# Optimization experiments

Hardware: AMD Instinct MI355X
Metric: run time of the kernel (lower is better)

The kernel has to match this reference:

```python
import jax, jax.numpy as jnp
import numpy as np

EPS = 1e-8  # torch F.cosine_similarity eps


def setup_inputs() -> dict:
    key = jax.random.key(0)
    ks = jax.random.split(key, 5)
    S, Q, D_in, D, N_WAY, K_SHOT = 100, 4096, 21168, 64, 20, 5
    return {
        "support_images": jax.random.normal(ks[0], (S, D_in), dtype=jnp.float32),
        "support_labels": jax.random.randint(ks[1], (S,), 0, N_WAY),
        "query_images": jax.random.normal(ks[2], (Q, D_in), dtype=jnp.float32),
        "n_way": N_WAY,
        "k_shot": K_SHOT,
        "backbone_w": jax.random.normal(ks[3], (D_in, D), dtype=jnp.float32) * 0.02,
        "backbone_b": jax.random.normal(ks[4], (D,), dtype=jnp.float32) * 0.02,
    }


def _l2_normalize(x):
    # matches torch cosine_similarity: x / max(||x||, eps)
    n = jnp.maximum(jnp.linalg.norm(x, axis=-1, keepdims=True), EPS)
    return x / n


def reference(support_images, support_labels, query_images, n_way, k_shot,
              backbone_w, backbone_b):
    # Backbone: linear embedding (stand-in for conv feature extractor)
    support_emb = support_images @ backbone_w + backbone_b   # [S, D]
    query_emb = query_images @ backbone_w + backbone_b       # [Q, D]

    # Cosine similarity between every query and every support sample: [Q, S]
    sims = _l2_normalize(query_emb) @ _l2_normalize(support_emb).T

    # Softmax over the support axis (per query), as in the original loop
    attn = jax.nn.softmax(sims, axis=1)                      # [Q, S]

    # Per-label scatter-add == one-hot segment-sum: [Q, n_way]
    one_hot = jax.nn.one_hot(support_labels, n_way, dtype=attn.dtype)  # [S, n_way]
    logits = attn @ one_hot
    return logits
```

## Files before the change

kernel.cpp:

```cpp
#include <hip/hip_runtime.h>
#include <hip/hip_bf16.h>
#include <math.h>

#define DEMB 64
#define BM   64
#define BKF  64
#define KSMAX 16

using short8 = __attribute__((ext_vector_type(8))) short;
using u16x8  = __attribute__((ext_vector_type(8))) unsigned short;
using f32x4  = __attribute__((ext_vector_type(4))) float;

__device__ __forceinline__ u16x8 cvt_bf8(float4 a0, float4 a1) {
    union { u16x8 s; __hip_bfloat16 h[8]; } u;
    u.h[0] = __float2bfloat16(a0.x);
    u.h[1] = __float2bfloat16(a0.y);
    u.h[2] = __float2bfloat16(a0.z);
    u.h[3] = __float2bfloat16(a0.w);
    u.h[4] = __float2bfloat16(a1.x);
    u.h[5] = __float2bfloat16(a1.y);
    u.h[6] = __float2bfloat16(a1.z);
    u.h[7] = __float2bfloat16(a1.w);
    return u.s;
}

__device__ __forceinline__ void gl16(const void* gsrc, void* lds) {
    __builtin_amdgcn_global_load_lds(
        (const __attribute__((address_space(1))) unsigned int*)gsrc,
        (__attribute__((address_space(3))) unsigned int*)lds,
        16, 0, 0);
}

__global__ __launch_bounds__(256) void prep_wt(
    const float* __restrict__ W, unsigned short* __restrict__ Wtk, int Din)
{
    const int t = blockIdx.x * 256 + threadIdx.x;
    const int oct = t >> 6, c = t & 63;
    union { u16x8 v; __hip_bfloat16 h[8]; } u;
    #pragma unroll
    for (int j = 0; j < 8; ++j) {
        int k = oct * 8 + j;
        float x = (k < Din) ? W[(size_t)k * DEMB + c] : 0.f;
        u.h[j] = __float2bfloat16(x);
    }
    *reinterpret_cast<u16x8*>(&Wtk[(size_t)t * 8]) = u.v;
}

__global__ __launch_bounds__(256) void gemm_mfma(
    const float* __restrict__ Xq, const float* __restrict__ Xs,
    const unsigned short* __restrict__ Wtk,
    float* __restrict__ qpart, float* __restrict__ spart,
    int Q, int S, int Din, int nQb, int cpk, int nbatch)
{
    __shared__ float          As[3][BM * BKF];
    __shared__ unsigned short Bs[3][8 * 64 * 8];

    const int tid  = threadIdx.x;
    const int wave = tid >> 6;
    const int lane = tid & 63;
    const int kg   = blockIdx.y;

    const bool isS = (int)blockIdx.x >= nQb;
    const float* X = isS ? Xs : Xq;
    const int nrows = isS ? S : Q;
    const int r0 = (isS ? ((int)blockIdx.x - nQb) : (int)blockIdx.x) * BM;
    float* part = isS ? spart : qpart;
    const int prow = isS ? 128 : Q;

    const int g  = lane >> 4;
    const int qp = lane & 15;

    const int col16 = lane & 15;
    const int frow  = 16 * wave + col16;
    const int fk    = (lane >> 4) * 8;

    f32x4 acc[4] = { {0.f,0.f,0.f,0.f}, {0.f,0.f,0.f,0.f},
                     {0.f,0.f,0.f,0.f}, {0.f,0.f,0.f,0.f} };

    const int b0 = kg * cpk;
    int b1 = b0 + cpk; if (b1 > nbatch) b1 = nbatch;

#define STAGE(SL, B) do {                                                      \
    const int kb_ = (B) * BKF;                                                 \
    _Pragma("unroll")                                                          \
    for (int i = 0; i < 4; ++i) {                                              \
        int rg_ = r0 + 16 * wave + 4 * i + g;                                  \
        if (rg_ >= nrows) rg_ = nrows - 1;                                     \
        const int q_ = qp ^ (4 * i + g);                                       \
        int kq_ = kb_ + 4 * q_;                                                \
        if (kq_ >= Din) kq_ = 0;                                               \
        gl16(X + (size_t)rg_ * Din + kq_,                                      \
             &As[SL][(16 * wave + 4 * i) * BKF]);                              \
    }                                                                          \
    _Pragma("unroll")                                                          \
    for (int j = 0; j < 2; ++j) {                                              \
        gl16(Wtk + ((size_t)((B) * 8 + 2 * wave + j) * 64 + lane) * 8,         \
             &Bs[SL][(2 * wave + j) * 512]);                                   \
    }                                                                          \
} while (0)

#define COMPUTE(SL, CC) do {                                                   \
    const int qa_ = (CC) * 8 + (fk >> 2);                                      \
    const float* Ab_ = &As[SL][frow * BKF];                                    \
    float4 fa_ = *reinterpret_cast<const float4*>(Ab_ + ((qa_    ) ^ col16) * 4); \
    float4 fb_ = *reinterpret_cast<const float4*>(Ab_ + ((qa_ + 1) ^ col16) * 4); \
    u16x8 afu_ = cvt_bf8(fa_, fb_);                                            \
    short8 af_ = (short8)afu_;                                                 \
    const int ob_ = ((CC) * 4 + (fk >> 3)) * 64;                               \
    short8 b0_ = *reinterpret_cast<const short8*>(&Bs[SL][(ob_ +  0 + col16) * 8]); \
    short8 b1_ = *reinterpret_cast<const short8*>(&Bs[SL][(ob_ + 16 + col16) * 8]); \
    short8 b2_ = *reinterpret_cast<const short8*>(&Bs[SL][(ob_ + 32 + col16) * 8]); \
    short8 b3_ = *reinterpret_cast<const short8*>(&Bs[SL][(ob_ + 48 + col16) * 8]); \
    acc[0] = __builtin_amdgcn_mfma_f32_16x16x32_bf16(af_, b0_, acc[0], 0, 0, 0);  \
    acc[1] = __builtin_amdgcn_mfma_f32_16x16x32_bf16(af_, b1_, acc[1], 0, 0, 0);  \
    acc[2] = __builtin_amdgcn_mfma_f32_16x16x32_bf16(af_, b2_, acc[2], 0, 0, 0);  \
    acc[3] = __builtin_amdgcn_mfma_f32_16x16x32_bf16(af_, b3_, acc[3], 0, 0, 0);  \
} while (0)

    STAGE(0, b0);
    if (b0 + 1 < b1) STAGE(1, b0 + 1);

    for (int b = b0; b < b1; ++b) {
        if (b + 1 < b1) asm volatile("s_waitcnt vmcnt(6)" ::: "memory");
        else            asm volatile("s_waitcnt vmcnt(0)" ::: "memory");
        __builtin_amdgcn_s_barrier();

        const int sl = (b - b0) % 3;
        if (b + 2 < b1) STAGE((sl + 2) % 3, b + 2);

        COMPUTE(sl, 0);
        COMPUTE(sl, 1);
    }

#undef STAGE
#undef COMPUTE

    #pragma unroll
    for (int cb = 0; cb < 4; ++cb) {
        #pragma unroll
        for (int i = 0; i < 4; ++i) {
            int row = r0 + 16 * wave + (lane >> 4) * 4 + i;
            if (row < nrows)
                part[((size_t)kg * prow + row) * DEMB + 16 * cb + col16] = acc[cb][i];
        }
    }
}

__global__ void support_finalize(const float* __restrict__ spart,
                                 const float* __restrict__ bias,
                                 float* __restrict__ sn, int S, int nkg)
{
    int s = blockIdx.x;
    int c = threadIdx.x;
    float e = bias[c];
    for (int g = 0; g < nkg; ++g)
        e += spart[((size_t)g * 128 + s) * DEMB + c];
    float ss = e * e;
    #pragma unroll
    for (int o = 32; o >= 1; o >>= 1) ss += __shfl_xor(ss, o, 64);
    sn[(size_t)s * DEMB + c] = e / fmaxf(sqrtf(ss), 1e-8f);
}

__global__ __launch_bounds__(256) void attend(
    const float* __restrict__ qpart, const float* __restrict__ sn_g,
    const float* __restrict__ bias, const int* __restrict__ labels,
    const int* __restrict__ p_nway, float* __restrict__ out,
    int S, int Q, int nkg)
{
    __shared__ float sn[100][65];
    __shared__ float qn[4][64];
    __shared__ float bins[4][32];
    __shared__ int   lab[100];

    const int tid  = threadIdx.x;
    const int w    = tid >> 6;
    const int lane = tid & 63;
    const int nw   = *p_nway;

    for (int i = tid; i < S * DEMB; i += 256) sn[i >> 6][i & 63] = sn_g[i];
    if (tid < S) lab[tid] = labels[tid];

    const int q = blockIdx.x * 4 + w;

    float e = bias[lane];
    for (int g = 0; g < nkg; ++g)
        e += qpart[((size_t)g * Q + q) * DEMB + lane];
    float ss = e * e;
    #pragma unroll
    for (int o = 32; o >= 1; o >>= 1) ss += __shfl_xor(ss, o, 64);
    e /= fmaxf(sqrtf(ss), 1e-8f);
    qn[w][lane] = e;
    if (lane < 32) bins[w][lane] = 0.f;
    __syncthreads();

    const bool v1 = (lane + 64) < S;
    const int  s1 = v1 ? lane + 64 : 0;
    float sim0 = 0.f, sim1 = 0.f;
    #pragma unroll 8
    for (int c = 0; c < DEMB; ++c) {
        float qc = qn[w][c];
        sim0 += qc * sn[lane][c];
        sim1 += qc * sn[s1][c];
    }
    if (!v1) sim1 = -INFINITY;

    float lm = fmaxf(sim0, sim1);
    #pragma unroll
    for (int o = 32; o >= 1; o >>= 1) lm = fmaxf(lm, __shfl_xor(lm, o, 64));
    float e0 = __expf(sim0 - lm);
    float e1 = v1 ? __expf(sim1 - lm) : 0.f;
    float d = e0 + e1;
    #pragma unroll
    for (int o = 32; o >= 1; o >>= 1) d += __shfl_xor(d, o, 64);

    atomicAdd(&bins[w][lab[lane]], e0);
    if (v1) atomicAdd(&bins[w][lab[s1]], e1);
    __syncthreads();

    if (lane < nw) out[(size_t)q * nw + lane] = bins[w][lane] / d;
}

extern "C" void kernel_launch(void* const* d_in, const int* in_sizes, int n_in,
                              void* d_out, int out_size, void* d_ws, size_t ws_size,
                              hipStream_t stream)
{
    const float* sup    = (const float*)d_in[0];
    const int*   labels = (const int*)d_in[1];
    const float* qry    = (const float*)d_in[2];
    const int*   p_nway = (const int*)d_in[3];
    const float* W      = (const float*)d_in[5];
    const float* bias   = (const float*)d_in[6];
    float* out = (float*)d_out;

    const int D   = DEMB;
    const int Din = in_sizes[5] / D;
    const int Q   = in_sizes[2] / Din;
    const int S   = in_sizes[1];

    const int nbatch = (Din + BKF - 1) / BKF;
    const int Koct   = nbatch * 8;

    char* wsb = (char*)d_ws;
    size_t wt_bytes = (size_t)Koct * 64 * 16;
    wt_bytes = (wt_bytes + 255) & ~(size_t)255;
    size_t sn_bytes = (size_t)S * D * sizeof(float);
    sn_bytes = (sn_bytes + 255) & ~(size_t)255;
    size_t per_ks = ((size_t)Q * D + 128 * D) * sizeof(float);

    size_t fixed = wt_bytes + sn_bytes;
    int ks = 1;
    if (ws_size > fixed + per_ks) {
        size_t avail = (ws_size - fixed) / per_ks;
        ks = (int)(avail < KSMAX ? avail : KSMAX);
        if (ks < 1) ks = 1;
    }
    const int cpk = (nbatch + ks - 1) / ks;
    const int nkg = (nbatch + cpk - 1) / cpk;

    unsigned short* Wtk = (unsigned short*)wsb;
    float* sn    = (float*)(wsb + wt_bytes);
    float* spart = (float*)(wsb + wt_bytes + sn_bytes);
    float* qpart = spart + (size_t)nkg * 128 * D;

    hipLaunchKernelGGL(prep_wt, dim3((Koct * 64) / 256), dim3(256), 0, stream,
                       W, Wtk, Din);

    const int nQb = (Q + BM - 1) / BM;
    const int nSb = (S + BM - 1) / BM;
    hipLaunchKernelGGL(gemm_mfma, dim3(nQb + nSb, nkg), dim3(256), 0, stream,
                       qry, sup, Wtk, qpart, spart, Q, S, Din, nQb, cpk, nbatch);

    hipLaunchKernelGGL(support_finalize, dim3(S), dim3(64), 0, stream,
                       spart, bias, sn, S, nkg);

    hipLaunchKernelGGL(attend, dim3(Q / 4), dim3(256), 0, stream,
                       qpart, sn, bias, labels, p_nway, out, S, Q, nkg);
}
```

Before: 117.7 us.

## Replace split-K GEMM with full-K 16-row tiles and fused normalization

The embedding GEMM no longer splits the reduction dimension across block groups with partial sums. Each block now owns 16 rows and runs the full K loop, with its two waves alternating K batches, then sums the two waves' results in LDS. Bias add and L2 normalization are fused into the GEMM epilogue, which removes the support_finalize kernel and the partial-sum reduction in attend. The trade-offs are fewer, smaller blocks (about 263 blocks of 128 threads), a long serial K loop per block, and each wave loading the full W tile by itself, which increases W traffic.

```diff
diff --git a/kernel.cpp b/kernel.cpp
--- a/kernel.cpp
+++ b/kernel.cpp
@@ -3,9 +3,8 @@
 #include <math.h>
 
 #define DEMB 64
-#define BM   64
+#define BM   16
 #define BKF  64
-#define KSMAX 16
 
 using short8 = __attribute__((ext_vector_type(8))) short;
 using u16x8  = __attribute__((ext_vector_type(8))) unsigned short;
@@ -46,126 +45,137 @@
     *reinterpret_cast<u16x8*>(&Wtk[(size_t)t * 8]) = u.v;
 }
 
-__global__ __launch_bounds__(256) void gemm_mfma(
+__global__ __launch_bounds__(128) void gemm_emb(
     const float* __restrict__ Xq, const float* __restrict__ Xs,
-    const unsigned short* __restrict__ Wtk,
-    float* __restrict__ qpart, float* __restrict__ spart,
-    int Q, int S, int Din, int nQb, int cpk, int nbatch)
-{
-    __shared__ float          As[3][BM * BKF];
-    __shared__ unsigned short Bs[3][8 * 64 * 8];
+    const unsigned short* __restrict__ Wtk, const float* __restrict__ bias,
+    float* __restrict__ qn, float* __restrict__ sn,
+    int Q, int S, int Din, int nQt, int nbatch)
+{
+    __shared__ float          As[2][3][BM * BKF];
+    __shared__ unsigned short Bs[2][3][8 * 64 * 8];
 
     const int tid  = threadIdx.x;
     const int wave = tid >> 6;
     const int lane = tid & 63;
-    const int kg   = blockIdx.y;
-
-    const bool isS = (int)blockIdx.x >= nQb;
+
+    const bool isS = (int)blockIdx.x >= nQt;
     const float* X = isS ? Xs : Xq;
     const int nrows = isS ? S : Q;
-    const int r0 = (isS ? ((int)blockIdx.x - nQb) : (int)blockIdx.x) * BM;
-    float* part = isS ? spart : qpart;
-    const int prow = isS ? 128 : Q;
+    const int r0 = (isS ? ((int)blockIdx.x - nQt) : (int)blockIdx.x) * BM;
+    float* dst = isS ? sn : qn;
 
     const int g  = lane >> 4;
     const int qp = lane & 15;
 
-    const int col16 = lane & 15;
-    const int frow  = 16 * wave + col16;
-    const int fk    = (lane >> 4) * 8;
+    const int c16 = lane & 15;
+    const int h   = lane >> 4;
 
     f32x4 acc[4] = { {0.f,0.f,0.f,0.f}, {0.f,0.f,0.f,0.f},
                      {0.f,0.f,0.f,0.f}, {0.f,0.f,0.f,0.f} };
-
-    const int b0 = kg * cpk;
-    int b1 = b0 + cpk; if (b1 > nbatch) b1 = nbatch;
 
 #define STAGE(SL, B) do {                                                      \
     const int kb_ = (B) * BKF;                                                 \
     _Pragma("unroll")                                                          \
     for (int i = 0; i < 4; ++i) {                                              \
-        int rg_ = r0 + 16 * wave + 4 * i + g;                                  \
+        const int rr_ = 4 * i + g;                                             \
+        int rg_ = r0 + rr_;                                                    \
         if (rg_ >= nrows) rg_ = nrows - 1;                                     \
-        const int q_ = qp ^ (4 * i + g);                                       \
+        const int q_ = qp ^ rr_;                                               \
         int kq_ = kb_ + 4 * q_;                                                \
         if (kq_ >= Din) kq_ = 0;                                               \
         gl16(X + (size_t)rg_ * Din + kq_,                                      \
-             &As[SL][(16 * wave + 4 * i) * BKF]);                              \
+             &As[wave][SL][(4 * i) * BKF]);                                    \
     }                                                                          \
     _Pragma("unroll")                                                          \
-    for (int j = 0; j < 2; ++j) {                                              \
-        gl16(Wtk + ((size_t)((B) * 8 + 2 * wave + j) * 64 + lane) * 8,         \
-             &Bs[SL][(2 * wave + j) * 512]);                                   \
+    for (int j = 0; j < 8; ++j) {                                              \
+        gl16(Wtk + ((size_t)((B) * 8 + j) * 64 + lane) * 8,                    \
+             &Bs[wave][SL][j * 512]);                                          \
     }                                                                          \
 } while (0)
 
 #define COMPUTE(SL, CC) do {                                                   \
-    const int qa_ = (CC) * 8 + (fk >> 2);                                      \
-    const float* Ab_ = &As[SL][frow * BKF];                                    \
-    float4 fa_ = *reinterpret_cast<const float4*>(Ab_ + ((qa_    ) ^ col16) * 4); \
-    float4 fb_ = *reinterpret_cast<const float4*>(Ab_ + ((qa_ + 1) ^ col16) * 4); \
-    u16x8 afu_ = cvt_bf8(fa_, fb_);                                            \
-    short8 af_ = (short8)afu_;                                                 \
-    const int ob_ = ((CC) * 4 + (fk >> 3)) * 64;                               \
-    short8 b0_ = *reinterpret_cast<const short8*>(&Bs[SL][(ob_ +  0 + col16) * 8]); \
-    short8 b1_ = *reinterpret_cast<const short8*>(&Bs[SL][(ob_ + 16 + col16) * 8]); \
-    short8 b2_ = *reinterpret_cast<const short8*>(&Bs[SL][(ob_ + 32 + col16) * 8]); \
-    short8 b3_ = *reinterpret_cast<const short8*>(&Bs[SL][(ob_ + 48 + col16) * 8]); \
+    const int qa_ = (CC) * 8 + 2 * h;                                          \
+    const float* Ab_ = &As[wave][SL][c16 * BKF];                               \
+    float4 fa_ = *reinterpret_cast<const float4*>(Ab_ + ((qa_    ) ^ c16) * 4);\
+    float4 fb_ = *reinterpret_cast<const float4*>(Ab_ + ((qa_ + 1) ^ c16) * 4);\
+    short8 af_ = (short8)cvt_bf8(fa_, fb_);                                    \
+    const int ob_ = ((CC) * 4 + h) * 64;                                       \
+    short8 b0_ = *reinterpret_cast<const short8*>(&Bs[wave][SL][(ob_ +  0 + c16) * 8]); \
+    short8 b1_ = *reinterpret_cast<const short8*>(&Bs[wave][SL][(ob_ + 16 + c16) * 8]); \
+    short8 b2_ = *reinterpret_cast<const short8*>(&Bs[wave][SL][(ob_ + 32 + c16) * 8]); \
+    short8 b3_ = *reinterpret_cast<const short8*>(&Bs[wave][SL][(ob_ + 48 + c16) * 8]); \
     acc[0] = __builtin_amdgcn_mfma_f32_16x16x32_bf16(af_, b0_, acc[0], 0, 0, 0);  \
     acc[1] = __builtin_amdgcn_mfma_f32_16x16x32_bf16(af_, b1_, acc[1], 0, 0, 0);  \
     acc[2] = __builtin_amdgcn_mfma_f32_16x16x32_bf16(af_, b2_, acc[2], 0, 0, 0);  \
     acc[3] = __builtin_amdgcn_mfma_f32_16x16x32_bf16(af_, b3_, acc[3], 0, 0, 0);  \
 } while (0)
 
-    STAGE(0, b0);
-    if (b0 + 1 < b1) STAGE(1, b0 + 1);
-
-    for (int b = b0; b < b1; ++b) {
-        if (b + 1 < b1) asm volatile("s_waitcnt vmcnt(6)" ::: "memory");
-        else            asm volatile("s_waitcnt vmcnt(0)" ::: "memory");
-        __builtin_amdgcn_s_barrier();
-
-        const int sl = (b - b0) % 3;
-        if (b + 2 < b1) STAGE((sl + 2) % 3, b + 2);
+    const int bw = wave;
+    STAGE(0, bw);
+    if (bw + 2 < nbatch) STAGE(1, bw + 2);
+    if (bw + 4 < nbatch) STAGE(2, bw + 4);
+
+    int sl = 0;
+    for (int bb = bw; bb < nbatch; bb += 2) {
+        if (bb + 4 < nbatch)      asm volatile("s_waitcnt vmcnt(24)" ::: "memory");
+        else if (bb + 2 < nbatch) asm volatile("s_waitcnt vmcnt(12)" ::: "memory");
+        else                      asm volatile("s_waitcnt vmcnt(0)"  ::: "memory");
 
         COMPUTE(sl, 0);
         COMPUTE(sl, 1);
+
+        asm volatile("s_waitcnt lgkmcnt(0)" ::: "memory");
+        __builtin_amdgcn_sched_barrier(0);
+
+        if (bb + 6 < nbatch) STAGE(sl, bb + 6);
+        sl = (sl == 2) ? 0 : sl + 1;
     }
 
 #undef STAGE
 #undef COMPUTE
 
-    #pragma unroll
-    for (int cb = 0; cb < 4; ++cb) {
+    __syncthreads();
+    float* red = &As[1][0][0];
+    if (wave == 1) {
+        #pragma unroll
+        for (int cb = 0; cb < 4; ++cb)
+            #pragma unroll
+            for (int i = 0; i < 4; ++i)
+                red[(4 * h + i) * 64 + 16 * cb + c16] = acc[cb][i];
+    }
+    __syncthreads();
+    if (wave == 0) {
+        float e[4][4], ss[4] = {0.f, 0.f, 0.f, 0.f};
+        #pragma unroll
+        for (int cb = 0; cb < 4; ++cb) {
+            float bv = bias[16 * cb + c16];
+            #pragma unroll
+            for (int i = 0; i < 4; ++i) {
+                e[cb][i] = acc[cb][i] + red[(4 * h + i) * 64 + 16 * cb + c16] + bv;
+                ss[i] += e[cb][i] * e[cb][i];
+            }
+        }
         #pragma unroll
         for (int i = 0; i < 4; ++i) {
-            int row = r0 + 16 * wave + (lane >> 4) * 4 + i;
-            if (row < nrows)
-                part[((size_t)kg * prow + row) * DEMB + 16 * cb + col16] = acc[cb][i];
+            #pragma unroll
+            for (int o = 1; o < 16; o <<= 1) ss[i] += __shfl_xor(ss[i], o, 64);
+            ss[i] = fmaxf(sqrtf(ss[i]), 1e-8f);
         }
-    }
-}
-
-__global__ void support_finalize(const float* __restrict__ spart,
-                                 const float* __restrict__ bias,
-                                 float* __restrict__ sn, int S, int nkg)
-{
-    int s = blockIdx.x;
-    int c = threadIdx.x;
-    float e = bias[c];
-    for (int g = 0; g < nkg; ++g)
-        e += spart[((size_t)g * 128 + s) * DEMB + c];
-    float ss = e * e;
-    #pragma unroll
-    for (int o = 32; o >= 1; o >>= 1) ss += __shfl_xor(ss, o, 64);
-    sn[(size_t)s * DEMB + c] = e / fmaxf(sqrtf(ss), 1e-8f);
+        #pragma unroll
+        for (int cb = 0; cb < 4; ++cb)
+            #pragma unroll
+            for (int i = 0; i < 4; ++i) {
+                int row = r0 + 4 * h + i;
+                if (row < nrows)
+                    dst[(size_t)row * DEMB + 16 * cb + c16] = e[cb][i] / ss[i];
+            }
+    }
 }
 
 __global__ __launch_bounds__(256) void attend(
-    const float* __restrict__ qpart, const float* __restrict__ sn_g,
-    const float* __restrict__ bias, const int* __restrict__ labels,
-    const int* __restrict__ p_nway, float* __restrict__ out,
-    int S, int Q, int nkg)
+    const float* __restrict__ qn_g, const float* __restrict__ sn_g,
+    const int* __restrict__ labels, const int* __restrict__ p_nway,
+    float* __restrict__ out, int S, int Q)
 {
     __shared__ float sn[100][65];
     __shared__ float qn[4][64];
@@ -181,15 +191,7 @@
     if (tid < S) lab[tid] = labels[tid];
 
     const int q = blockIdx.x * 4 + w;
-
-    float e = bias[lane];
-    for (int g = 0; g < nkg; ++g)
-        e += qpart[((size_t)g * Q + q) * DEMB + lane];
-    float ss = e * e;
-    #pragma unroll
-    for (int o = 32; o >= 1; o >>= 1) ss += __shfl_xor(ss, o, 64);
-    e /= fmaxf(sqrtf(ss), 1e-8f);
-    qn[w][lane] = e;
+    qn[w][lane] = qn_g[(size_t)q * DEMB + lane];
     if (lane < 32) bins[w][lane] = 0.f;
     __syncthreads();
 
@@ -243,36 +245,21 @@
     char* wsb = (char*)d_ws;
     size_t wt_bytes = (size_t)Koct * 64 * 16;
     wt_bytes = (wt_bytes + 255) & ~(size_t)255;
-    size_t sn_bytes = (size_t)S * D * sizeof(float);
-    sn_bytes = (sn_bytes + 255) & ~(size_t)255;
-    size_t per_ks = ((size_t)Q * D + 128 * D) * sizeof(float);
-
-    size_t fixed = wt_bytes + sn_bytes;
-    int ks = 1;
-    if (ws_size > fixed + per_ks) {
-        size_t avail = (ws_size - fixed) / per_ks;
-        ks = (int)(avail < KSMAX ? avail : KSMAX);
-        if (ks < 1) ks = 1;
-    }
-    const int cpk = (nbatch + ks - 1) / ks;
-    const int nkg = (nbatch + cpk - 1) / cpk;
+    size_t qn_bytes = (size_t)Q * D * sizeof(float);
+    qn_bytes = (qn_bytes + 255) & ~(size_t)255;
 
     unsigned short* Wtk = (unsigned short*)wsb;
-    float* sn    = (float*)(wsb + wt_bytes);
-    float* spart = (float*)(wsb + wt_bytes + sn_bytes);
-    float* qpart = spart + (size_t)nkg * 128 * D;
+    float* qn = (float*)(wsb + wt_bytes);
+    float* sn = (float*)(wsb + wt_bytes + qn_bytes);
 
     hipLaunchKernelGGL(prep_wt, dim3((Koct * 64) / 256), dim3(256), 0, stream,
                        W, Wtk, Din);
 
-    const int nQb = (Q + BM - 1) / BM;
-    const int nSb = (S + BM - 1) / BM;
-    hipLaunchKernelGGL(gemm_mfma, dim3(nQb + nSb, nkg), dim3(256), 0, stream,
-                       qry, sup, Wtk, qpart, spart, Q, S, Din, nQb, cpk, nbatch);
-
-    hipLaunchKernelGGL(support_finalize, dim3(S), dim3(64), 0, stream,
-                       spart, bias, sn, S, nkg);
+    const int nQt = (Q + BM - 1) / BM;
+    const int nSt = (S + BM - 1) / BM;
+    hipLaunchKernelGGL(gemm_emb, dim3(nQt + nSt), dim3(128), 0, stream,
+                       qry, sup, Wtk, bias, qn, sn, Q, S, Din, nQt, nbatch);
 
     hipLaunchKernelGGL(attend, dim3(Q / 4), dim3(256), 0, stream,
-                       qpart, sn, bias, labels, p_nway, out, S, Q, nkg);
-}
+                       qn, sn, labels, p_nway, out, S, Q);
+}
```

New measurement: 214.4 us. 1.82x slower.
